# Performance work log

Hardware: AMD Instinct MI355X
Metric: run time of the kernel (lower is better)

## Reference

```python
import jax, jax.numpy as jnp
import numpy as np

B, T, E, H, V = 128, 20, 512, 512, 10000


def setup_inputs() -> dict:
    key = jax.random.key(0)
    ks = jax.random.split(key, 8)
    s = 0.1  # uniform init range used by init_weights()
    k = 1.0 / np.sqrt(H)  # default torch LSTM init scale
    return {
        "features": jax.random.normal(ks[0], (B, E), jnp.float32),
        "captions": jax.random.randint(ks[1], (B, T), 0, V, jnp.int32),
        "h0": jnp.zeros((B, H), jnp.float32),
        "c0": jnp.zeros((B, H), jnp.float32),
        "embed_w": jax.random.uniform(ks[2], (V, E), jnp.float32, -s, s),
        "W_ih": jax.random.uniform(ks[3], (4 * H, E), jnp.float32, -k, k),
        "W_hh": jax.random.uniform(ks[4], (4 * H, H), jnp.float32, -k, k),
        "b_ih": jax.random.uniform(ks[5], (4 * H,), jnp.float32, -k, k),
        "b_hh": jax.random.uniform(ks[6], (4 * H,), jnp.float32, -k, k),
        "W_lin": jax.random.uniform(ks[7], (V, H), jnp.float32, -s, s),
        "b_lin": jnp.zeros((V,), jnp.float32),
        "maxlen": T,
    }


def reference(features, captions, h0, c0, embed_w, W_ih, W_hh, b_ih, b_hh,
              W_lin, b_lin, maxlen):
    # Teacher-forced decode (MCRollouts=False branch):
    # step 0 input is the image feature; step t>0 input is embed(captions[:, t-1]).
    xs = jnp.concatenate(
        [features[:, None, :], embed_w[captions[:, : maxlen - 1]]], axis=1
    )  # [B, T, E]

    def step(carry, x):
        h, c = carry
        gates = x @ W_ih.T + b_ih + h @ W_hh.T + b_hh  # [B, 4H]
        i, f, g, o = jnp.split(gates, 4, axis=-1)  # PyTorch gate order i,f,g,o
        i = jax.nn.sigmoid(i)
        f = jax.nn.sigmoid(f)
        g = jnp.tanh(g)
        o = jax.nn.sigmoid(o)
        c = f * c + i * g
        h = o * jnp.tanh(c)
        logits = h @ W_lin.T + b_lin  # [B, V]
        return (h, c), logits

    _, logits = jax.lax.scan(step, (h0, c0), xs.transpose(1, 0, 2))  # [T, B, V]
    # All lengths equal maxlen, so pack_padded_sequence(batch_first=True)[0]
    # is the time-major flatten: [T*B, V].
    return logits.reshape(maxlen * features.shape[0], -1)
```

## Files before the change

kernel.cpp:

```cpp
#include <hip/hip_runtime.h>
#include <math.h>

#define BB 128
#define TT 20
#define EE 512
#define HH 512
#define VV 10000
#define G4 2048
#define NBLK 64

typedef __attribute__((ext_vector_type(8))) short     bf16x8;
typedef __attribute__((ext_vector_type(4))) float     f32x4;
typedef __attribute__((ext_vector_type(8))) unsigned short u16x8;

static __device__ __forceinline__ unsigned short f2bf(float f) {
    union { float f; unsigned u; } v; v.f = f;
    const unsigned u = v.u;
    return (unsigned short)((u + 0x7FFFu + ((u >> 16) & 1u)) >> 16);
}
static __device__ __forceinline__ float bf2f(unsigned short h) {
    union { unsigned u; float f; } v; v.u = ((unsigned)h) << 16;
    return v.f;
}

__global__ __launch_bounds__(256) void cvt_bf16(
    const float* __restrict__ in, unsigned short* __restrict__ out, int n)
{
    const int i = (blockIdx.x * 256 + threadIdx.x) * 8;
    if (i >= n) return;
    const float4 a = *(const float4*)(in + i);
    const float4 b = *(const float4*)(in + i + 4);
    u16x8 o;
    o[0] = f2bf(a.x); o[1] = f2bf(a.y); o[2] = f2bf(a.z); o[3] = f2bf(a.w);
    o[4] = f2bf(b.x); o[5] = f2bf(b.y); o[6] = f2bf(b.z); o[7] = f2bf(b.w);
    *(u16x8*)(out + i) = o;
}

__global__ __launch_bounds__(256) void cvt_bf16_hilo(
    const float* __restrict__ in,
    unsigned short* __restrict__ hi, unsigned short* __restrict__ lo, int n)
{
    const int i = (blockIdx.x * 256 + threadIdx.x) * 8;
    if (i >= n) return;
    u16x8 oh, ol;
    #pragma unroll
    for (int j = 0; j < 8; ++j) {
        const float x = in[i + j];
        const unsigned short h = f2bf(x);
        oh[j] = h;
        ol[j] = f2bf(x - bf2f(h));
    }
    *(u16x8*)(hi + i) = oh;
    *(u16x8*)(lo + i) = ol;
}

__global__ __launch_bounds__(128) void gather_x16(
    const float* __restrict__ features,
    const int* __restrict__ captions,
    const float* __restrict__ embed_w,
    unsigned short* __restrict__ X16)
{
    const int r = blockIdx.x;
    const int t = r >> 7;
    const int b = r & 127;
    const float* src;
    if (t == 0) src = features + (size_t)b * EE;
    else        src = embed_w + (size_t)captions[b * TT + (t - 1)] * EE;
    const float4 v = ((const float4*)src)[threadIdx.x];
    ushort4 o;
    o.x = f2bf(v.x); o.y = f2bf(v.y); o.z = f2bf(v.z); o.w = f2bf(v.w);
    ((ushort4*)(X16 + (size_t)r * EE))[threadIdx.x] = o;
}

__global__ __launch_bounds__(256) void gemm_bf16_mfma(
    const unsigned short* __restrict__ A,
    const unsigned short* __restrict__ Bm,
    const float* __restrict__ bias0,
    const float* __restrict__ bias1,
    float* __restrict__ C,
    int M, int N)
{
    __shared__ unsigned short As[128][40];
    __shared__ unsigned short Bs[128][40];

    const int m0  = blockIdx.y * 128;
    const int n0  = blockIdx.x * 128;
    const int tid = threadIdx.x;
    const int wave = tid >> 6;
    const int lane = tid & 63;
    const int wr = wave >> 1, wc = wave & 1;
    const int l15 = lane & 15, l4 = lane >> 4;

    f32x4 acc[4][4] = {};

    const int srow = tid >> 2;
    const int sch  = (tid & 3) * 8;

    for (int k0 = 0; k0 < 512; k0 += 32) {
        #pragma unroll
        for (int p = 0; p < 2; ++p) {
            const int r = srow + p * 64;
            {
                const uint4 v = *(const uint4*)(A + (size_t)(m0 + r) * 512 + k0 + sch);
                *(uint4*)&As[r][sch] = v;
            }
            {
                const int nrow = n0 + r;
                uint4 v = make_uint4(0u, 0u, 0u, 0u);
                if (nrow < N)
                    v = *(const uint4*)(Bm + (size_t)nrow * 512 + k0 + sch);
                *(uint4*)&Bs[r][sch] = v;
            }
        }
        __syncthreads();

        bf16x8 af[4], bfr[4];
        #pragma unroll
        for (int i = 0; i < 4; ++i)
            af[i] = *(const bf16x8*)&As[wr * 64 + i * 16 + l15][l4 * 8];
        #pragma unroll
        for (int i = 0; i < 4; ++i)
            bfr[i] = *(const bf16x8*)&Bs[wc * 64 + i * 16 + l15][l4 * 8];

        #pragma unroll
        for (int i = 0; i < 4; ++i)
            #pragma unroll
            for (int j = 0; j < 4; ++j)
                acc[i][j] = __builtin_amdgcn_mfma_f32_16x16x32_bf16(
                    af[i], bfr[j], acc[i][j], 0, 0, 0);
        __syncthreads();
    }

    #pragma unroll
    for (int j = 0; j < 4; ++j) {
        const int col = n0 + wc * 64 + j * 16 + l15;
        if (col >= N) continue;
        float bv = 0.f;
        if (bias0) bv += bias0[col];
        if (bias1) bv += bias1[col];
        #pragma unroll
        for (int i = 0; i < 4; ++i) {
            const int row = m0 + wr * 64 + i * 16 + l4 * 4;
            #pragma unroll
            for (int r = 0; r < 4; ++r)
                C[(size_t)(row + r) * N + col] = acc[i][j][r] + bv;
        }
    }
}

__global__ void init_bar(int* __restrict__ bar) {
    if (threadIdx.x < 2 * TT) bar[threadIdx.x] = 0;
}

__global__ __launch_bounds__(512, 1) void lstm_fused_mfma2(
    const float* __restrict__ c0,
    const float* __restrict__ Xp,
    const unsigned short* __restrict__ Whi,
    const unsigned short* __restrict__ Wlo,
    unsigned short* __restrict__ Hhi,
    unsigned short* __restrict__ Hlo,
    int* __restrict__ bar)
{
    __shared__ unsigned short hsH[2][64][72];
    __shared__ unsigned short hsL[2][64][72];
    __shared__ float gsh[4][64][17];

    const int blk   = blockIdx.x;
    const int mhalf = blk >> 5;
    const int n0    = (blk & 31) * 16;
    const int tid   = threadIdx.x;
    const int w     = tid >> 6;
    const int lane  = tid & 63;
    const int l15   = lane & 15, l4 = lane >> 4;
    const int gate  = w & 3;
    const int mh2   = w >> 2;

    bf16x8 whi[16], wlo[16];
    {
        const size_t wrow = (size_t)(gate * 512 + n0 + l15) * 512;
        #pragma unroll
        for (int kk = 0; kk < 16; ++kk) {
            whi[kk] = *(const bf16x8*)(Whi + wrow + kk * 32 + l4 * 8);
            wlo[kk] = *(const bf16x8*)(Wlo + wrow + kk * 32 + l4 * 8);
        }
    }

    const int srow = tid >> 3;
    const int sseg = (tid & 7) * 8;

    const int arow = tid >> 2;
    const int aq   = (tid & 3) * 4;

    f32x4 creg = {};
    if (tid < 256)
        creg = *(const f32x4*)(c0 + (size_t)(mhalf * 64 + arow) * 512 + n0 + aq);

    for (int t = 0; t < TT; ++t) {
        const size_t abase = ((size_t)t * 128 + mhalf * 64) * 512;
        const size_t srcrow = abase + (size_t)srow * 512;

        {
            const uint4 rh = *(const uint4*)(Hhi + srcrow + sseg);
            const uint4 rl = *(const uint4*)(Hlo + srcrow + sseg);
            *(uint4*)&hsH[0][srow][sseg] = rh;
            *(uint4*)&hsL[0][srow][sseg] = rl;
        }

        f32x4 acc[2] = {};
        #pragma unroll
        for (int c = 0; c < 8; ++c) {
            __syncthreads();
            uint4 nh = {}, nl = {};
            if (c < 7) {
                nh = *(const uint4*)(Hhi + srcrow + (c + 1) * 64 + sseg);
                nl = *(const uint4*)(Hlo + srcrow + (c + 1) * 64 + sseg);
            }
            const int buf = c & 1;
            #pragma unroll
            for (int kkl = 0; kkl < 2; ++kkl) {
                const int kkg = c * 2 + kkl;
                #pragma unroll
                for (int mi = 0; mi < 2; ++mi) {
                    const int r = mh2 * 32 + mi * 16 + l15;
                    const bf16x8 ah = *(const bf16x8*)&hsH[buf][r][kkl * 32 + l4 * 8];
                    const bf16x8 al = *(const bf16x8*)&hsL[buf][r][kkl * 32 + l4 * 8];
                    acc[mi] = __builtin_amdgcn_mfma_f32_16x16x32_bf16(ah, whi[kkg], acc[mi], 0, 0, 0);
                    acc[mi] = __builtin_amdgcn_mfma_f32_16x16x32_bf16(al, whi[kkg], acc[mi], 0, 0, 0);
                    acc[mi] = __builtin_amdgcn_mfma_f32_16x16x32_bf16(ah, wlo[kkg], acc[mi], 0, 0, 0);
                }
            }
            if (c < 7) {
                *(uint4*)&hsH[buf ^ 1][srow][sseg] = nh;
                *(uint4*)&hsL[buf ^ 1][srow][sseg] = nl;
            }
        }

        #pragma unroll
        for (int mi = 0; mi < 2; ++mi)
            #pragma unroll
            for (int r = 0; r < 4; ++r)
                gsh[gate][mh2 * 32 + mi * 16 + l4 * 4 + r][l15] = acc[mi][r];
        __syncthreads();

        if (tid < 256) {
            const size_t xrow = ((size_t)t * 128 + mhalf * 64 + arow) * (size_t)G4;
            const float4 xi = *(const float4*)(Xp + xrow + 0 * 512 + n0 + aq);
            const float4 xf = *(const float4*)(Xp + xrow + 1 * 512 + n0 + aq);
            const float4 xg = *(const float4*)(Xp + xrow + 2 * 512 + n0 + aq);
            const float4 xo = *(const float4*)(Xp + xrow + 3 * 512 + n0 + aq);
            const float gxi[4] = {xi.x, xi.y, xi.z, xi.w};
            const float gxf[4] = {xf.x, xf.y, xf.z, xf.w};
            const float gxg[4] = {xg.x, xg.y, xg.z, xg.w};
            const float gxo[4] = {xo.x, xo.y, xo.z, xo.w};
            ushort4 hh4, hl4;
            unsigned short* ph = (unsigned short*)&hh4;
            unsigned short* pl = (unsigned short*)&hl4;
            #pragma unroll
            for (int j = 0; j < 4; ++j) {
                const float gi = gsh[0][arow][aq + j] + gxi[j];
                const float gf = gsh[1][arow][aq + j] + gxf[j];
                const float gg = gsh[2][arow][aq + j] + gxg[j];
                const float go = gsh[3][arow][aq + j] + gxo[j];
                const float iv = 1.f / (1.f + expf(-gi));
                const float fv = 1.f / (1.f + expf(-gf));
                const float gv = tanhf(gg);
                const float ov = 1.f / (1.f + expf(-go));
                creg[j] = fv * creg[j] + iv * gv;
                const float hv = ov * tanhf(creg[j]);
                const unsigned short h16 = f2bf(hv);
                ph[j] = h16;
                pl[j] = f2bf(hv - bf2f(h16));
            }
            const size_t ho = ((size_t)(t + 1) * 128 + mhalf * 64 + arow) * 512 + n0 + aq;
            *(ushort4*)(Hhi + ho) = hh4;
            *(ushort4*)(Hlo + ho) = hl4;
        }

        __syncthreads();
        if (t < TT - 1) {
            if (tid == 0) {
                int* slot = bar + mhalf * TT + t;
                __hip_atomic_fetch_add(slot, 1, __ATOMIC_RELEASE, __HIP_MEMORY_SCOPE_AGENT);
                while (__hip_atomic_load(slot, __ATOMIC_RELAXED, __HIP_MEMORY_SCOPE_AGENT) < 32)
                    __builtin_amdgcn_s_sleep(2);
                (void)__hip_atomic_load(slot, __ATOMIC_ACQUIRE, __HIP_MEMORY_SCOPE_AGENT);
            }
            __syncthreads();
        }
    }
}

extern "C" void kernel_launch(void* const* d_in, const int* in_sizes, int n_in,
                              void* d_out, int out_size, void* d_ws, size_t ws_size,
                              hipStream_t stream)
{
    const float* features = (const float*)d_in[0];
    const int*   captions = (const int*)d_in[1];
    const float* h0       = (const float*)d_in[2];
    const float* c0       = (const float*)d_in[3];
    const float* embed_w  = (const float*)d_in[4];
    const float* W_ih     = (const float*)d_in[5];
    const float* W_hh     = (const float*)d_in[6];
    const float* b_ih     = (const float*)d_in[7];
    const float* b_hh     = (const float*)d_in[8];
    const float* W_lin    = (const float*)d_in[9];
    const float* b_lin    = (const float*)d_in[10];
    float* out = (float*)d_out;

    char* p = (char*)d_ws;
    unsigned short* X16    = (unsigned short*)p; p += (size_t)2560 * 512 * 2;
    unsigned short* Wih16  = (unsigned short*)p; p += (size_t)2048 * 512 * 2;
    unsigned short* Wlin16 = (unsigned short*)p; p += (size_t)10000 * 512 * 2;
    unsigned short* WhhHi  = (unsigned short*)p; p += (size_t)2048 * 512 * 2;
    unsigned short* WhhLo  = (unsigned short*)p; p += (size_t)2048 * 512 * 2;
    unsigned short* Hhi    = (unsigned short*)p; p += (size_t)(TT + 1) * 128 * 512 * 2;
    unsigned short* Hlo    = (unsigned short*)p; p += (size_t)(TT + 1) * 128 * 512 * 2;
    float*          Xp     = (float*)p;          p += (size_t)2560 * 2048 * 4;
    int*            bar    = (int*)p;            p += 256;

    cvt_bf16<<<dim3(512),  dim3(256), 0, stream>>>(W_ih, Wih16, 2048 * 512);
    cvt_bf16<<<dim3(2500), dim3(256), 0, stream>>>(W_lin, Wlin16, 10000 * 512);
    cvt_bf16_hilo<<<dim3(512), dim3(256), 0, stream>>>(W_hh, WhhHi, WhhLo, 2048 * 512);
    cvt_bf16_hilo<<<dim3(32),  dim3(256), 0, stream>>>(h0, Hhi, Hlo, 128 * 512);
    gather_x16<<<dim3(TT * BB), dim3(128), 0, stream>>>(features, captions, embed_w, X16);

    gemm_bf16_mfma<<<dim3(G4 / 128, (TT * BB) / 128), dim3(256), 0, stream>>>(
        X16, Wih16, b_ih, b_hh, Xp, TT * BB, G4);

    init_bar<<<dim3(1), dim3(64), 0, stream>>>(bar);
    lstm_fused_mfma2<<<dim3(NBLK), dim3(512), 0, stream>>>(
        c0, Xp, WhhHi, WhhLo, Hhi, Hlo, bar);

    gemm_bf16_mfma<<<dim3((VV + 127) / 128, (TT * BB) / 128), dim3(256), 0, stream>>>(
        Hhi + (size_t)128 * 512, Wlin16, b_lin, nullptr, out, TT * BB, VV);
}
```

Measured before the change: 452.8 us.

## Stage whole hidden state in swizzled LDS and use per-block flag barrier

The recurrent LSTM kernel now loads the full 64x512 hi/lo hidden-state tile into a 128KB XOR-swizzled LDS buffer in one pass with a single barrier. This replaces the 8-chunk double-buffered loop that synchronised on every chunk. MFMA work is split across two independent accumulator chains, and the Xp gate-input loads are hoisted before the matmul to hide their latency. The grid barrier now uses per-block flags polled by a wavefront with a ballot instead of a shared atomic counter, and fast exp-based sigmoid/tanh replace expf/tanhf. The trade-offs are very large LDS use and slightly lower transcendental accuracy.

```diff
diff --git a/kernel.cpp b/kernel.cpp
--- a/kernel.cpp
+++ b/kernel.cpp
@@ -21,6 +21,15 @@
 static __device__ __forceinline__ float bf2f(unsigned short h) {
     union { unsigned u; float f; } v; v.u = ((unsigned)h) << 16;
     return v.f;
+}
+static __device__ __forceinline__ float sigm_fast(float x) {
+    return 1.f / (1.f + __expf(-x));
+}
+static __device__ __forceinline__ float tanh_fast(float x) {
+    const float ax = fabsf(x);
+    const float e  = __expf(2.f * ax);
+    const float t  = 1.f - 2.f / (e + 1.f);
+    return copysignf(t, x);
 }
 
 __global__ __launch_bounds__(256) void cvt_bf16(
@@ -148,26 +157,30 @@
     }
 }
 
-__global__ void init_bar(int* __restrict__ bar) {
-    if (threadIdx.x < 2 * TT) bar[threadIdx.x] = 0;
-}
-
-__global__ __launch_bounds__(512, 1) void lstm_fused_mfma2(
+__global__ __launch_bounds__(512) void init_flags(int* __restrict__ flags) {
+    for (int i = threadIdx.x; i < 2 * TT * 32; i += 512) flags[i] = 0;
+}
+
+#define HS_IDX(row, col) ((((row) << 9) + (col)) ^ (((row) & 7) << 3))
+
+__global__ __launch_bounds__(512, 1) void lstm_fused_mfma3(
     const float* __restrict__ c0,
     const float* __restrict__ Xp,
     const unsigned short* __restrict__ Whi,
     const unsigned short* __restrict__ Wlo,
     unsigned short* __restrict__ Hhi,
     unsigned short* __restrict__ Hlo,
-    int* __restrict__ bar)
-{
-    __shared__ unsigned short hsH[2][64][72];
-    __shared__ unsigned short hsL[2][64][72];
-    __shared__ float gsh[4][64][17];
+    int* __restrict__ flags)
+{
+    __shared__ char smem[131072];
+    unsigned short* hsH = (unsigned short*)smem;
+    unsigned short* hsL = hsH + 64 * 512;
+    float* gsh = (float*)smem;
 
     const int blk   = blockIdx.x;
     const int mhalf = blk >> 5;
-    const int n0    = (blk & 31) * 16;
+    const int ntile = blk & 31;
+    const int n0    = ntile * 16;
     const int tid   = threadIdx.x;
     const int w     = tid >> 6;
     const int lane  = tid & 63;
@@ -185,8 +198,8 @@
         }
     }
 
-    const int srow = tid >> 3;
-    const int sseg = (tid & 7) * 8;
+    const int srow  = tid >> 3;
+    const int scol0 = (tid & 7) * 8;
 
     const int arow = tid >> 2;
     const int aq   = (tid & 3) * 4;
@@ -197,57 +210,62 @@
 
     for (int t = 0; t < TT; ++t) {
         const size_t abase = ((size_t)t * 128 + mhalf * 64) * 512;
-        const size_t srcrow = abase + (size_t)srow * 512;
-
-        {
-            const uint4 rh = *(const uint4*)(Hhi + srcrow + sseg);
-            const uint4 rl = *(const uint4*)(Hlo + srcrow + sseg);
-            *(uint4*)&hsH[0][srow][sseg] = rh;
-            *(uint4*)&hsL[0][srow][sseg] = rl;
-        }
-
-        f32x4 acc[2] = {};
-        #pragma unroll
-        for (int c = 0; c < 8; ++c) {
-            __syncthreads();
-            uint4 nh = {}, nl = {};
-            if (c < 7) {
-                nh = *(const uint4*)(Hhi + srcrow + (c + 1) * 64 + sseg);
-                nl = *(const uint4*)(Hlo + srcrow + (c + 1) * 64 + sseg);
-            }
-            const int buf = c & 1;
-            #pragma unroll
-            for (int kkl = 0; kkl < 2; ++kkl) {
-                const int kkg = c * 2 + kkl;
-                #pragma unroll
-                for (int mi = 0; mi < 2; ++mi) {
-                    const int r = mh2 * 32 + mi * 16 + l15;
-                    const bf16x8 ah = *(const bf16x8*)&hsH[buf][r][kkl * 32 + l4 * 8];
-                    const bf16x8 al = *(const bf16x8*)&hsL[buf][r][kkl * 32 + l4 * 8];
-                    acc[mi] = __builtin_amdgcn_mfma_f32_16x16x32_bf16(ah, whi[kkg], acc[mi], 0, 0, 0);
-                    acc[mi] = __builtin_amdgcn_mfma_f32_16x16x32_bf16(al, whi[kkg], acc[mi], 0, 0, 0);
-                    acc[mi] = __builtin_amdgcn_mfma_f32_16x16x32_bf16(ah, wlo[kkg], acc[mi], 0, 0, 0);
-                }
-            }
-            if (c < 7) {
-                *(uint4*)&hsH[buf ^ 1][srow][sseg] = nh;
-                *(uint4*)&hsL[buf ^ 1][srow][sseg] = nl;
-            }
-        }
-
-        #pragma unroll
-        for (int mi = 0; mi < 2; ++mi)
-            #pragma unroll
-            for (int r = 0; r < 4; ++r)
-                gsh[gate][mh2 * 32 + mi * 16 + l4 * 4 + r][l15] = acc[mi][r];
-        __syncthreads();
-
+
+        float4 xi, xf, xg, xo;
         if (tid < 256) {
             const size_t xrow = ((size_t)t * 128 + mhalf * 64 + arow) * (size_t)G4;
-            const float4 xi = *(const float4*)(Xp + xrow + 0 * 512 + n0 + aq);
-            const float4 xf = *(const float4*)(Xp + xrow + 1 * 512 + n0 + aq);
-            const float4 xg = *(const float4*)(Xp + xrow + 2 * 512 + n0 + aq);
-            const float4 xo = *(const float4*)(Xp + xrow + 3 * 512 + n0 + aq);
+            xi = *(const float4*)(Xp + xrow + 0 * 512 + n0 + aq);
+            xf = *(const float4*)(Xp + xrow + 1 * 512 + n0 + aq);
+            xg = *(const float4*)(Xp + xrow + 2 * 512 + n0 + aq);
+            xo = *(const float4*)(Xp + xrow + 3 * 512 + n0 + aq);
+        }
+
+        {
+            const unsigned short* gH = Hhi + abase + (size_t)srow * 512;
+            const unsigned short* gL = Hlo + abase + (size_t)srow * 512;
+            #pragma unroll
+            for (int s = 0; s < 8; ++s) {
+                const int col = scol0 + s * 64;
+                const uint4 vh = *(const uint4*)(gH + col);
+                const uint4 vl = *(const uint4*)(gL + col);
+                *(uint4*)&hsH[HS_IDX(srow, col)] = vh;
+                *(uint4*)&hsL[HS_IDX(srow, col)] = vl;
+            }
+        }
+        __syncthreads();
+
+        f32x4 a0[2] = {}, a1[2] = {};
+        #pragma unroll
+        for (int kk = 0; kk < 8; ++kk) {
+            #pragma unroll
+            for (int mi = 0; mi < 2; ++mi) {
+                const int r  = mh2 * 32 + mi * 16 + l15;
+                const int cA = kk * 32 + l4 * 8;
+                const int cB = (kk + 8) * 32 + l4 * 8;
+                const bf16x8 ahA = *(const bf16x8*)&hsH[HS_IDX(r, cA)];
+                const bf16x8 alA = *(const bf16x8*)&hsL[HS_IDX(r, cA)];
+                const bf16x8 ahB = *(const bf16x8*)&hsH[HS_IDX(r, cB)];
+                const bf16x8 alB = *(const bf16x8*)&hsL[HS_IDX(r, cB)];
+                a0[mi] = __builtin_amdgcn_mfma_f32_16x16x32_bf16(ahA, whi[kk],     a0[mi], 0, 0, 0);
+                a0[mi] = __builtin_amdgcn_mfma_f32_16x16x32_bf16(alA, whi[kk],     a0[mi], 0, 0, 0);
+                a0[mi] = __builtin_amdgcn_mfma_f32_16x16x32_bf16(ahA, wlo[kk],     a0[mi], 0, 0, 0);
+                a1[mi] = __builtin_amdgcn_mfma_f32_16x16x32_bf16(ahB, whi[kk + 8], a1[mi], 0, 0, 0);
+                a1[mi] = __builtin_amdgcn_mfma_f32_16x16x32_bf16(alB, whi[kk + 8], a1[mi], 0, 0, 0);
+                a1[mi] = __builtin_amdgcn_mfma_f32_16x16x32_bf16(ahB, wlo[kk + 8], a1[mi], 0, 0, 0);
+            }
+        }
+        __syncthreads();
+
+        #pragma unroll
+        for (int mi = 0; mi < 2; ++mi) {
+            const f32x4 acc = a0[mi] + a1[mi];
+            #pragma unroll
+            for (int r = 0; r < 4; ++r)
+                gsh[gate * 1088 + (mh2 * 32 + mi * 16 + l4 * 4 + r) * 17 + l15] = acc[r];
+        }
+        __syncthreads();
+
+        if (tid < 256) {
             const float gxi[4] = {xi.x, xi.y, xi.z, xi.w};
             const float gxf[4] = {xf.x, xf.y, xf.z, xf.w};
             const float gxg[4] = {xg.x, xg.y, xg.z, xg.w};
@@ -257,16 +275,16 @@
             unsigned short* pl = (unsigned short*)&hl4;
             #pragma unroll
             for (int j = 0; j < 4; ++j) {
-                const float gi = gsh[0][arow][aq + j] + gxi[j];
-                const float gf = gsh[1][arow][aq + j] + gxf[j];
-                const float gg = gsh[2][arow][aq + j] + gxg[j];
-                const float go = gsh[3][arow][aq + j] + gxo[j];
-                const float iv = 1.f / (1.f + expf(-gi));
-                const float fv = 1.f / (1.f + expf(-gf));
-                const float gv = tanhf(gg);
-                const float ov = 1.f / (1.f + expf(-go));
+                const float gi = gsh[0 * 1088 + arow * 17 + aq + j] + gxi[j];
+                const float gf = gsh[1 * 1088 + arow * 17 + aq + j] + gxf[j];
+                const float gg = gsh[2 * 1088 + arow * 17 + aq + j] + gxg[j];
+                const float go = gsh[3 * 1088 + arow * 17 + aq + j] + gxo[j];
+                const float iv = sigm_fast(gi);
+                const float fv = sigm_fast(gf);
+                const float gv = tanh_fast(gg);
+                const float ov = sigm_fast(go);
                 creg[j] = fv * creg[j] + iv * gv;
-                const float hv = ov * tanhf(creg[j]);
+                const float hv = ov * tanh_fast(creg[j]);
                 const unsigned short h16 = f2bf(hv);
                 ph[j] = h16;
                 pl[j] = f2bf(hv - bf2f(h16));
@@ -276,14 +294,20 @@
             *(ushort4*)(Hlo + ho) = hl4;
         }
 
-        __syncthreads();
         if (t < TT - 1) {
-            if (tid == 0) {
-                int* slot = bar + mhalf * TT + t;
-                __hip_atomic_fetch_add(slot, 1, __ATOMIC_RELEASE, __HIP_MEMORY_SCOPE_AGENT);
-                while (__hip_atomic_load(slot, __ATOMIC_RELAXED, __HIP_MEMORY_SCOPE_AGENT) < 32)
-                    __builtin_amdgcn_s_sleep(2);
-                (void)__hip_atomic_load(slot, __ATOMIC_ACQUIRE, __HIP_MEMORY_SCOPE_AGENT);
+            __syncthreads();
+            int* base = flags + (mhalf * TT + t) * 32;
+            if (tid == 0)
+                __hip_atomic_store(base + ntile, 1, __ATOMIC_RELEASE, __HIP_MEMORY_SCOPE_AGENT);
+            if (tid < 64) {
+                const int myf = lane & 31;
+                while (true) {
+                    const int v = __hip_atomic_load(base + myf, __ATOMIC_RELAXED, __HIP_MEMORY_SCOPE_AGENT);
+                    if (__ballot(v != 0) == ~0ull) break;
+                    __builtin_amdgcn_s_sleep(1);
+                }
+                if (lane == 0)
+                    (void)__hip_atomic_load(base, __ATOMIC_ACQUIRE, __HIP_MEMORY_SCOPE_AGENT);
             }
             __syncthreads();
         }
@@ -316,7 +340,7 @@
     unsigned short* Hhi    = (unsigned short*)p; p += (size_t)(TT + 1) * 128 * 512 * 2;
     unsigned short* Hlo    = (unsigned short*)p; p += (size_t)(TT + 1) * 128 * 512 * 2;
     float*          Xp     = (float*)p;          p += (size_t)2560 * 2048 * 4;
-    int*            bar    = (int*)p;            p += 256;
+    int*            flags  = (int*)p;            p += 2 * TT * 32 * 4;
 
     cvt_bf16<<<dim3(512),  dim3(256), 0, stream>>>(W_ih, Wih16, 2048 * 512);
     cvt_bf16<<<dim3(2500), dim3(256), 0, stream>>>(W_lin, Wlin16, 10000 * 512);
@@ -327,9 +351,9 @@
     gemm_bf16_mfma<<<dim3(G4 / 128, (TT * BB) / 128), dim3(256), 0, stream>>>(
         X16, Wih16, b_ih, b_hh, Xp, TT * BB, G4);
 
-    init_bar<<<dim3(1), dim3(64), 0, stream>>>(bar);
-    lstm_fused_mfma2<<<dim3(NBLK), dim3(512), 0, stream>>>(
-        c0, Xp, WhhHi, WhhLo, Hhi, Hlo, bar);
+    init_flags<<<dim3(1), dim3(512), 0, stream>>>(flags);
+    lstm_fused_mfma3<<<dim3(NBLK), dim3(512), 0, stream>>>(
+        c0, Xp, WhhHi, WhhLo, Hhi, Hlo, flags);
 
     gemm_bf16_mfma<<<dim3((VV + 127) / 128, (TT * BB) / 128), dim3(256), 0, stream>>>(
         Hhi + (size_t)128 * 512, Wlin16, b_lin, nullptr, out, TT * BB, VV);
```

After: 424.6 us. 6.2% less time.
